# Kernel tuning notes

Measured on AMD Instinct MI355X. Metric: run time of the kernel, lower is better.

Reference implementation:

```python
import jax, jax.numpy as jnp
import numpy as np

B, IN_DIM, D, H, L = 16, 4096, 100, 200, 4
N, E = B * IN_DIM, 8 * B * IN_DIM
EPS = 1e-7  # GENConv message eps


def setup_inputs() -> dict:
    key = jax.random.key(0)
    ks = jax.random.split(key, 16)
    s = 0.05
    return {
        "x": jax.random.normal(ks[0], (N, 1), jnp.float32),
        "edge_index": jax.random.randint(ks[1], (2, E), 0, N),
        "batch_ids": jnp.repeat(jnp.arange(B), IN_DIM),  # graphs of exactly IN_DIM nodes
        "enc_w": jax.random.normal(ks[2], (1, D), jnp.float32) * s,
        "enc_b": jnp.zeros((D,), jnp.float32),
        "h1_w": jax.random.normal(ks[3], (IN_DIM, 1000), jnp.float32) * 0.02,
        "h1_b": jnp.zeros((1000,), jnp.float32),
        "h2_w": jax.random.normal(ks[4], (1000, 100), jnp.float32) * s,
        "h2_b": jnp.zeros((100,), jnp.float32),
        "ln_g": jnp.ones((L, D), jnp.float32),
        "ln_b": jnp.zeros((L, D), jnp.float32),
        "w1": jax.random.normal(ks[5], (L, D, H), jnp.float32) * s,
        "b1": jnp.zeros((L, H), jnp.float32),
        "bn_g": jnp.ones((L, H), jnp.float32),
        "bn_b": jnp.zeros((L, H), jnp.float32),
        "w2": jax.random.normal(ks[6], (L, H, D), jnp.float32) * s,
        "b2": jnp.zeros((L, D), jnp.float32),
        "dec_w": jax.random.normal(ks[7], (D, 1), jnp.float32) * s,
        "dec_b": jnp.zeros((1,), jnp.float32),
    }


def reference(x, edge_index, batch_ids, enc_w, enc_b, h1_w, h1_b, h2_w, h2_b,
              ln_g, ln_b, w1, b1, bn_g, bn_b, w2, b2, dec_w, dec_b):
    src, dst = edge_index[0], edge_index[1]
    # dense branch: [B, IN_DIM] -> 1000 -> 100 with leaky_relu (dropout p=0)
    xs = x.reshape(B, IN_DIM)
    xs = jax.nn.leaky_relu(xs @ h1_w + h1_b, 0.01)
    xs = jax.nn.leaky_relu(xs @ h2_w + h2_b, 0.01)

    h = x @ enc_w + enc_b  # node encoder -> [N, D]
    for i in range(L):  # DeepGCNLayer res+: x + GENConv(dropout(relu(LN(x))))
        mu = jnp.mean(h, axis=-1, keepdims=True)
        var = jnp.mean((h - mu) ** 2, axis=-1, keepdims=True)
        hn = (h - mu) * jax.lax.rsqrt(var + 1e-5) * ln_g[i] + ln_b[i]
        hn = jnp.maximum(hn, 0.0)  # act (dropout in eval mode = identity)
        # GENConv: message = relu(x_j) + eps, softmax aggregation (t=1)
        m = jnp.maximum(hn[src], 0.0) + EPS            # [E, D]
        mx = jax.ops.segment_max(m, dst, num_segments=N)
        ex = jnp.exp(m - mx[dst])
        den = jax.ops.segment_sum(ex, dst, num_segments=N)
        agg = jax.ops.segment_sum((ex / den[dst]) * m, dst, num_segments=N)
        # out = mlp(agg + x): Linear(D,2D) -> BN(eval) -> ReLU -> Linear(2D,D)
        z = (agg + hn) @ w1[i] + b1[i]
        z = jnp.maximum(z * bn_g[i] + bn_b[i], 0.0)
        h = h + (z @ w2[i] + b2[i])

    pooled = jax.ops.segment_sum(h, batch_ids, num_segments=B) / IN_DIM
    out = 0.5 * xs + 0.5 * pooled
    return (out @ dec_w + dec_b)[:, 0]
```

## Files before the change

kernel.cpp:

```cpp
#include <hip/hip_runtime.h>
#include <hip/hip_bf16.h>
#include <hip/hip_fp16.h>
#include <math.h>

#define B_ 16
#define IN_DIM_ 4096
#define D_ 100
#define H_ 200
#define L_ 4
#define N_ (B_*IN_DIM_)
#define E_ (8*B_*IN_DIM_)
#define EPS_ 1e-7f

typedef __attribute__((ext_vector_type(8))) short bf16x8s;
typedef __attribute__((ext_vector_type(4))) float f32x4;

__device__ inline unsigned pack_bf16x2(float a, float b){
  __hip_bfloat16 x = __float2bfloat16(a), y = __float2bfloat16(b);
  unsigned short ux = *(unsigned short*)&x, uy = *(unsigned short*)&y;
  return (unsigned)ux | ((unsigned)uy << 16);
}
__device__ inline __half2 u2h(unsigned v){ return *(__half2*)&v; }

__device__ inline unsigned char f2fp8(float v){
  unsigned p = __builtin_amdgcn_cvt_pk_fp8_f32(v, 0.f, 0u, false);
  return (unsigned char)(p & 0xFF);
}

__global__ void enc_stats_kernel(const float* __restrict__ enc_w,
                                 const float* __restrict__ enc_b,
                                 float* __restrict__ stats) {
  __shared__ float sw[128], sb[128], sww[128], swb[128], sbb[128];
  int t = threadIdx.x;
  float w=0.f, b=0.f;
  if (t < D_){ w = enc_w[t]; b = enc_b[t]; }
  sw[t]=w; sb[t]=b; sww[t]=w*w; swb[t]=w*b; sbb[t]=b*b;
  __syncthreads();
  for (int off=64; off; off>>=1){
    if (t<off){ sw[t]+=sw[t+off]; sb[t]+=sb[t+off]; sww[t]+=sww[t+off];
                swb[t]+=swb[t+off]; sbb[t]+=sbb[t+off]; }
    __syncthreads();
  }
  if (t==0){
    float mw = sw[0]*(1.f/D_), mb = sb[0]*(1.f/D_);
    stats[0]=mw; stats[1]=mb;
    stats[2]=sww[0]*(1.f/D_) - mw*mw;
    stats[3]=swb[0]*(1.f/D_) - mw*mb;
    stats[4]=sbb[0]*(1.f/D_) - mb*mb;
  }
}

#define D1_BLKS_   512
#define ENC_BLKS_  2048
#define DEG_BLKS_  2048
#define PREP_BLKS_ 448
#define SETUP_BLKS_ (D1_BLKS_+ENC_BLKS_+DEG_BLKS_+PREP_BLKS_)

__global__ void setup_kernel(const float* __restrict__ x, const float* __restrict__ enc_w,
                             const float* __restrict__ enc_b, const float* __restrict__ g0,
                             const float* __restrict__ b0, const float* __restrict__ stats,
                             __half* __restrict__ h, char* __restrict__ hnb,
                             char* __restrict__ hnb8,
                             const int* __restrict__ dsts, int* __restrict__ deg,
                             const float* __restrict__ h1_w, float* __restrict__ xs1acc,
                             const float* __restrict__ w1, const float* __restrict__ w2,
                             __hip_bfloat16* __restrict__ w1T, char* __restrict__ w2T8) {
  __shared__ float xl[16][32];
  int bid = blockIdx.x;
  int t = threadIdx.x;
  if (bid < D1_BLKS_) {
    int bx = bid & 3, by = bid >> 2;
    int k0 = by * 32;
    for (int i = t; i < 16*32; i += 256) {
      int b = i >> 5, kk = i & 31;
      xl[b][kk] = x[b*IN_DIM_ + k0 + kk];
    }
    __syncthreads();
    int c = bx*256 + t;
    if (c >= 1000) return;
    float acc[B_];
    #pragma unroll
    for (int b=0;b<B_;b++) acc[b]=0.f;
    #pragma unroll 4
    for (int kk=0; kk<32; kk++) {
      float w = h1_w[(size_t)(k0+kk)*1000 + c];
      #pragma unroll
      for (int b=0;b<B_;b++) acc[b] += xl[b][kk]*w;
    }
    #pragma unroll
    for (int b=0;b<B_;b++) atomicAdd(&xs1acc[b*1000+c], acc[b]);
  } else if (bid < D1_BLKS_+ENC_BLKS_) {
    int eb = bid - D1_BLKS_;
    int wave = t >> 6, lane = t & 63;
    int base = eb*32 + wave*8;
    float mw = stats[0], mb = stats[1], vw = stats[2], cwb = stats[3], vb = stats[4];
    float xv = 0.f;
    if (lane < 8) xv = x[base + lane];
    int c0 = 2*lane, c1 = c0+1;
    bool v = c0 < D_;
    float ew0=0.f, ew1=0.f, ebv0=0.f, ebv1=0.f, gg0=0.f, gg1=0.f, bv0=0.f, bv1=0.f;
    if (v) { ew0=enc_w[c0]; ew1=enc_w[c1]; ebv0=enc_b[c0]; ebv1=enc_b[c1];
             gg0=g0[c0]; gg1=g0[c1]; bv0=b0[c0]; bv1=b0[c1]; }
    #pragma unroll
    for (int it=0; it<8; ++it) {
      int wid = base + it;
      float xn = __shfl(xv, it, 64);
      float mu = fmaf(xn, mw, mb);
      float var = fmaf(xn*xn, vw, fmaf(2.f*xn, cwb, vb));
      float rstd = rsqrtf(var + 1e-5f);
      float h0 = fmaf(xn, ew0, ebv0);
      float h1 = fmaf(xn, ew1, ebv1);
      if (c0 < 112) *(__half2*)&h[(size_t)wid*112 + c0] = __floats2half2_rn(h0, h1);
      float n0 = v? fmaxf(fmaf((h0-mu)*rstd, gg0, bv0), 0.f) : 0.f;
      float n1 = v? fmaxf(fmaf((h1-mu)*rstd, gg1, bv1), 0.f) : 0.f;
      *(__half2*)(hnb + (size_t)wid*256 + 4*lane) = __floats2half2_rn(n0, n1);
      unsigned short p8 = (unsigned short)f2fp8(n0) | ((unsigned short)f2fp8(n1) << 8);
      *(unsigned short*)(hnb8 + (size_t)wid*128 + c0) = p8;
    }
  } else if (bid < D1_BLKS_+ENC_BLKS_+DEG_BLKS_) {
    int e = (bid - (D1_BLKS_+ENC_BLKS_))*256 + t;
    if (e < E_) atomicAdd(&deg[dsts[e]], 1);
  } else {
    int idx = (bid - (D1_BLKS_+ENC_BLKS_+DEG_BLKS_))*256 + t;
    if (idx < L_*224*128) {
      int l = idx / (224*128);
      int rem = idx % (224*128);
      int col = rem / 128, k = rem % 128;
      float v = (col < H_ && k < D_) ? w1[(l*D_ + k)*H_ + col] : 0.f;
      w1T[idx] = __float2bfloat16(v);
    }
    if (idx < L_*112*224) {
      int l = idx / (112*224);
      int rem = idx % (112*224);
      int col = rem / 224, k = rem % 224;
      float v = (col < D_ && k < H_) ? w2[(l*H_ + k)*D_ + col] : 0.f;
      w2T8[idx] = f2fp8(v);
    }
  }
}

__global__ void stage2_kernel(const int* __restrict__ deg, int* __restrict__ row_start,
                              const float* __restrict__ xs1acc, const float* __restrict__ h1_b,
                              const float* __restrict__ h2_w, float* __restrict__ xs2acc,
                              int* __restrict__ hist) {
  __shared__ int sums[1024];
  int t = threadIdx.x;
  int bid = blockIdx.x;
  if (bid == 0) {
    int base = t*64;
    int s = 0;
    for (int j=0;j<64;j++) s += deg[base+j];
    sums[t] = s;
    __syncthreads();
    for (int off=1; off<1024; off<<=1){
      int add = (t>=off)? sums[t-off] : 0;
      __syncthreads();
      sums[t] += add;
      __syncthreads();
    }
    int excl = (t==0)? 0 : sums[t-1];
    int run = excl;
    for (int j=0;j<64;j++){ row_start[base+j] = run; run += deg[base+j]; }
    if (t==1023) row_start[N_] = run;
  } else if (bid <= 4) {
    int T = (bid-1)*1024 + t;
    if (T >= 100*40) return;
    int c = T % 100, kc = T / 100;
    int k0 = kc*25;
    float acc[B_];
    #pragma unroll
    for (int b=0;b<B_;b++) acc[b]=0.f;
    for (int kk=0;kk<25;kk++){
      int k = k0+kk;
      float w = h2_w[k*100 + c];
      float bk = h1_b[k];
      #pragma unroll
      for (int b=0;b<B_;b++){
        float m = xs1acc[b*1000+k] + bk;
        m = (m>0.f)? m : 0.01f*m;
        acc[b] += m*w;
      }
    }
    #pragma unroll
    for (int b=0;b<B_;b++) atomicAdd(&xs2acc[b*100+c], acc[b]);
  } else {
    __shared__ int lh[256];
    if (t < 256) lh[t] = 0;
    __syncthreads();
    int base = (bid-5)*16384;
    for (int n = base + t; n < base + 16384; n += 1024) {
      int d = deg[n]; if (d > 255) d = 255;
      atomicAdd(&lh[d], 1);
    }
    __syncthreads();
    if (t < 256 && lh[t] > 0) atomicAdd(&hist[t], lh[t]);
  }
}

__global__ void binscan_kernel(const int* __restrict__ hist, int* __restrict__ binoff,
                               int* __restrict__ bincnt) {
  __shared__ int s[256];
  int t = threadIdx.x;
  int hv = hist[t];
  s[t] = hv;
  __syncthreads();
  for (int off=1; off<256; off<<=1){
    int v = (t>=off)? s[t-off] : 0;
    __syncthreads();
    s[t] += v;
    __syncthreads();
  }
  binoff[t] = s[t] - hv;
  bincnt[t] = 0;
}

__global__ void scatter_kernel(const int* __restrict__ srcs, const int* __restrict__ dst,
                               const int* __restrict__ row_start, int* __restrict__ cnt,
                               int* __restrict__ sorted_src,
                               const int* __restrict__ deg, const int* __restrict__ binoff,
                               int* __restrict__ bincnt, int* __restrict__ order) {
  int bid = blockIdx.x;
  int t = threadIdx.x;
  if (bid < 2048) {
    int e = bid*256 + t;
    int d = dst[e];
    int p = row_start[d] + atomicAdd(&cnt[d], 1);
    sorted_src[p] = srcs[e];
  } else {
    __shared__ int lh[256], lbase[256];
    int n = (bid-2048)*256 + t;
    int d = deg[n]; int b = (d > 255) ? 255 : d;
    lh[t] = 0;
    __syncthreads();
    int myrank = atomicAdd(&lh[b], 1);
    __syncthreads();
    lbase[t] = (lh[t] > 0) ? atomicAdd(&bincnt[t], lh[t]) : 0;
    __syncthreads();
    order[binoff[b] + lbase[b] + myrank] = n;
  }
}

__global__ void agg_kernel(const char* __restrict__ hnb, const char* __restrict__ hnb8,
                           const int* __restrict__ row_start,
                           const int* __restrict__ sorted_src,
                           const int* __restrict__ order, unsigned* __restrict__ u) {
  int gw = (blockIdx.x*256 + threadIdx.x) >> 6;
  int lane = threadIdx.x & 63;
  int lpos = lane & 31;
  int gbase = lane & 32;
  int node = order[gw*2 + (lane >> 5)];
  int beg = row_start[node];
  int deg = row_start[node+1] - beg;
  int dother = __shfl_xor(deg, 32, 64);
  int mdeg = deg > dother ? deg : dother;
  const char* lanep8 = hnb8 + 4*lpos;
  float s0=0.f,s1=0.f,s2=0.f,s3=0.f, w0=0.f,w1=0.f,w2=0.f,w3=0.f;

#define CONSUME_(R) { \
    float v0=__builtin_amdgcn_cvt_f32_fp8(R,0)+EPS_; \
    float v1=__builtin_amdgcn_cvt_f32_fp8(R,1)+EPS_; \
    float v2=__builtin_amdgcn_cvt_f32_fp8(R,2)+EPS_; \
    float v3=__builtin_amdgcn_cvt_f32_fp8(R,3)+EPS_; \
    float e0=__expf(v0), e1=__expf(v1), e2=__expf(v2), e3=__expf(v3); \
    s0+=e0; w0=fmaf(e0,v0,w0); s1+=e1; w1=fmaf(e1,v1,w1); \
    s2+=e2; w2=fmaf(e2,v2,w2); s3+=e3; w3=fmaf(e3,v3,w3); }

  for (int cb=0; cb<mdeg; cb+=32){
    int cidx = (cb + lpos < deg) ? sorted_src[beg + cb + lpos] : 0;
    int cnt = mdeg - cb; if (cnt > 32) cnt = 32;
    int grem = deg - cb;
    int glim = grem < cnt ? grem : cnt; if (glim < 0) glim = 0;
    unsigned r0=0, r1=0, r2=0, r3=0;
    if (0 < glim) r0 = *(const unsigned*)(lanep8 + (size_t)__shfl(cidx, gbase+0)*128);
    if (1 < glim) r1 = *(const unsigned*)(lanep8 + (size_t)__shfl(cidx, gbase+1)*128);
    if (2 < glim) r2 = *(const unsigned*)(lanep8 + (size_t)__shfl(cidx, gbase+2)*128);
    if (3 < glim) r3 = *(const unsigned*)(lanep8 + (size_t)__shfl(cidx, gbase+3)*128);
    for (int j=0; j<cnt; j+=4){
      unsigned n0=0, n1=0, n2=0, n3=0;
      if (j+4 < glim) n0 = *(const unsigned*)(lanep8 + (size_t)__shfl(cidx, gbase+j+4)*128);
      if (j+5 < glim) n1 = *(const unsigned*)(lanep8 + (size_t)__shfl(cidx, gbase+j+5)*128);
      if (j+6 < glim) n2 = *(const unsigned*)(lanep8 + (size_t)__shfl(cidx, gbase+j+6)*128);
      if (j+7 < glim) n3 = *(const unsigned*)(lanep8 + (size_t)__shfl(cidx, gbase+j+7)*128);
      if (j   < glim) CONSUME_(r0);
      if (j+1 < glim) CONSUME_(r1);
      if (j+2 < glim) CONSUME_(r2);
      if (j+3 < glim) CONSUME_(r3);
      r0=n0; r1=n1; r2=n2; r3=n3;
    }
  }
#undef CONSUME_

  uint2 own = *(const uint2*)(hnb + (size_t)node*256 + 8*lpos);
  __half2 oa = u2h(own.x), ob = u2h(own.y);
  float u0 = ((deg>0)? w0/s0 : 0.f) + __low2float(oa);
  float u1 = ((deg>0)? w1/s1 : 0.f) + __high2float(oa);
  float u2 = ((deg>0)? w2/s2 : 0.f) + __low2float(ob);
  float u3 = ((deg>0)? w3/s3 : 0.f) + __high2float(ob);
  if (lpos >= 25) { u0=0.f; u1=0.f; u2=0.f; u3=0.f; }
  uint2 outv; outv.x = pack_bf16x2(u0,u1); outv.y = pack_bf16x2(u2,u3);
  *(uint2*)((char*)u + (size_t)node*256 + 8*lpos) = outv;
}

__global__ __launch_bounds__(256,4) void gemm1_kernel(
    const char* __restrict__ u, const __hip_bfloat16* __restrict__ w1T,
    const float* __restrict__ b1, const float* __restrict__ bng, const float* __restrict__ bnb,
    char* __restrict__ z8) {
  __shared__ __align__(16) char wL[112*272];
  int bid = blockIdx.x;
  int half = bid & 1;
  size_t row0 = (size_t)(bid >> 1) * 64;
  int t = threadIdx.x;
  const char* wg = (const char*)w1T + (size_t)half*112*256;
  #pragma unroll
  for (int c = t; c < 1792; c += 256) {
    int r = c >> 4, sb = (c & 15) << 4;
    *(float4*)(wL + r*272 + sb) = *(const float4*)(wg + (size_t)r*256 + sb);
  }
  __syncthreads();
  int wave = t >> 6, lane = t & 63;
  int l15 = lane & 15;
  int kgb = (lane >> 4) << 4;
  int ar = wave*16 + l15;
  bf16x8s a[4];
  #pragma unroll
  for (int ks=0; ks<4; ks++)
    a[ks] = *(const bf16x8s*)(u + (row0 + ar)*256 + ks*64 + kgb);
  f32x4 acc[7];
  #pragma unroll
  for (int n=0;n<7;n++) acc[n] = (f32x4){0.f,0.f,0.f,0.f};
  #pragma unroll
  for (int ks=0; ks<4; ks++) {
    int kb = ks*64 + kgb;
    #pragma unroll
    for (int n=0;n<7;n++) {
      bf16x8s b = *(const bf16x8s*)(wL + (n*16 + l15)*272 + kb);
      acc[n] = __builtin_amdgcn_mfma_f32_16x16x32_bf16(a[ks], b, acc[n], 0, 0, 0);
    }
  }
  size_t rbase = row0 + wave*16 + ((lane>>4)<<2);
  #pragma unroll
  for (int n=0;n<7;n++) {
    int col = half*112 + n*16 + l15;
    float bias = (col < H_) ? b1[col] : 0.f;
    float g    = (col < H_) ? bng[col] : 0.f;
    float bb   = (col < H_) ? bnb[col] : 0.f;
    #pragma unroll
    for (int r=0;r<4;r++) {
      float v = fmaxf((acc[n][r] + bias)*g + bb, 0.f);
      if (col >= H_) v = 0.f;
      *(unsigned char*)(z8 + (rbase + r)*224 + col) = f2fp8(v);
    }
  }
}

template<int LAST>
__global__ __launch_bounds__(256,4) void gemm2_kernel(
    const char* __restrict__ z8, const char* __restrict__ w2T8,
    const float* __restrict__ b2, __half* __restrict__ h,
    const float* __restrict__ lng, const float* __restrict__ lnb,
    char* __restrict__ hnb, char* __restrict__ hnb8, float* __restrict__ pooled) {
  __shared__ __align__(16) char wL[112*232];
  int t = threadIdx.x;
  size_t row0 = (size_t)blockIdx.x * 64;
  const char* wg = w2T8;
  for (int c = t; c < 1568; c += 256) {
    int r = c / 14, sb = (c - r*14) << 4;
    *(float4*)(wL + r*232 + sb) = *(const float4*)(wg + (size_t)r*224 + sb);
  }
  __syncthreads();
  int wave = t >> 6, lane = t & 63;
  int l15 = lane & 15;
  int g8 = (lane >> 4) << 3;
  int ar = wave*16 + l15;
  long long av[7];
  {
    const char* zrow = z8 + (row0 + ar)*224;
    #pragma unroll
    for (int ks=0; ks<7; ks++)
      av[ks] = *(const long long*)(zrow + ks*32 + g8);
  }
  f32x4 acc[7];
  #pragma unroll
  for (int n=0;n<7;n++) acc[n] = (f32x4){0.f,0.f,0.f,0.f};
  #pragma unroll
  for (int ks=0; ks<7; ks++) {
    int kb = ks*32 + g8;
    #pragma unroll
    for (int n=0;n<7;n++) {
      long long bv = *(const long long*)(wL + (n*16 + l15)*232 + kb);
      acc[n] = __builtin_amdgcn_mfma_f32_16x16x32_fp8_fp8(av[ks], bv, acc[n], 0, 0, 0);
    }
  }
  size_t rbase = row0 + wave*16 + ((lane>>4)<<2);

  float x_[7][4];
  float sum[4]  = {0,0,0,0};
  float sum2[4] = {0,0,0,0};
  float psum[7] = {0,0,0,0,0,0,0};
  #pragma unroll
  for (int n=0;n<7;n++) {
    int col = n*16 + l15;
    bool valid = col < D_;
    float bias = valid ? b2[col] : 0.f;
    #pragma unroll
    for (int r=0;r<4;r++) {
      float xv = 0.f;
      if (valid) xv = acc[n][r] + bias + __half2float(h[(rbase + r)*112 + col]);
      x_[n][r] = xv;
      if (LAST) {
        psum[n] += xv;
      } else {
        sum[r] += xv; sum2[r] += xv*xv;
        if (valid) h[(rbase + r)*112 + col] = __float2half(xv);
      }
    }
  }

  if (LAST) {
    #pragma unroll
    for (int n=0;n<7;n++) {
      psum[n] += __shfl_xor(psum[n], 16, 64);
      psum[n] += __shfl_xor(psum[n], 32, 64);
    }
    __syncthreads();
    float* ps = (float*)wL;
    if (lane < 16) {
      #pragma unroll
      for (int n=0;n<7;n++) ps[wave*112 + n*16 + l15] = psum[n];
    }
    __syncthreads();
    if (t < D_) {
      float v = ps[t] + ps[112+t] + ps[224+t] + ps[336+t];
      int b = (int)(row0 >> 12);
      atomicAdd(&pooled[b*D_ + t], v);
    }
  } else {
    #pragma unroll
    for (int r=0;r<4;r++) {
      float s = sum[r], s2 = sum2[r];
      #pragma unroll
      for (int m=1;m<16;m<<=1) { s += __shfl_xor(s, m, 16); s2 += __shfl_xor(s2, m, 16); }
      sum[r] = s; sum2[r] = s2;
    }
    #pragma unroll
    for (int n=0;n<7;n++) {
      int col = n*16 + l15;
      float g  = (col < D_) ? lng[col] : 0.f;
      float be = (col < D_) ? lnb[col] : 0.f;
      #pragma unroll
      for (int r=0;r<4;r++) {
        float mu = sum[r]*(1.f/D_);
        float var = sum2[r]*(1.f/D_) - mu*mu;
        float rstd = rsqrtf(var + 1e-5f);
        float hv = fmaxf(fmaf((x_[n][r]-mu)*rstd, g, be), 0.f);
        if (col >= D_) hv = 0.f;
        *(__half*)(hnb + (rbase + r)*256 + 2*col) = __float2half(hv);
        *(unsigned char*)(hnb8 + (rbase + r)*128 + col) = f2fp8(hv);
      }
    }
    {
      int col = 112 + l15;
      __half zh = __float2half(0.f);
      #pragma unroll
      for (int r=0;r<4;r++) {
        *(__half*)(hnb + (rbase + r)*256 + 2*col) = zh;
        *(unsigned char*)(hnb8 + (rbase + r)*128 + col) = 0;
      }
    }
  }
}

__global__ void final_kernel(const float* __restrict__ xs2acc, const float* __restrict__ h2_b,
                             const float* __restrict__ pooled,
                             const float* __restrict__ dec_w, const float* __restrict__ dec_b,
                             float* __restrict__ out) {
  __shared__ float red[128];
  int t = threadIdx.x;
  for (int b=0;b<B_;b++){
    float v = 0.f;
    if (t < D_) {
      float xs = xs2acc[b*D_+t] + h2_b[t];
      xs = (xs>0.f)? xs : 0.01f*xs;
      v = (0.5f*xs + (0.5f/IN_DIM_)*pooled[b*D_+t]) * dec_w[t];
    }
    red[t] = v;
    __syncthreads();
    for (int off=64; off; off>>=1){
      if (t < off) red[t] += red[t+off];
      __syncthreads();
    }
    if (t==0) out[b] = red[0] + dec_b[0];
    __syncthreads();
  }
}

extern "C" void kernel_launch(void* const* d_in, const int* in_sizes, int n_in,
                              void* d_out, int out_size, void* d_ws, size_t ws_size,
                              hipStream_t stream) {
  const float* x      = (const float*)d_in[0];
  const int*   eidx   = (const int*)d_in[1];
  const float* enc_w  = (const float*)d_in[3];
  const float* enc_b  = (const float*)d_in[4];
  const float* h1_w   = (const float*)d_in[5];
  const float* h1_b   = (const float*)d_in[6];
  const float* h2_w   = (const float*)d_in[7];
  const float* h2_b   = (const float*)d_in[8];
  const float* ln_g   = (const float*)d_in[9];
  const float* ln_b   = (const float*)d_in[10];
  const float* w1     = (const float*)d_in[11];
  const float* b1     = (const float*)d_in[12];
  const float* bn_g   = (const float*)d_in[13];
  const float* bn_b   = (const float*)d_in[14];
  const float* w2     = (const float*)d_in[15];
  const float* b2     = (const float*)d_in[16];
  const float* dec_w  = (const float*)d_in[17];
  const float* dec_b  = (const float*)d_in[18];
  float* out = (float*)d_out;

  char* ws = (char*)d_ws;
  size_t off = 0;
  auto alloc = [&](size_t bytes)->char* {
    char* p = ws + off;
    off += (bytes + 255) & ~(size_t)255;
    return p;
  };
  __half* h     = (__half*)alloc((size_t)N_*112*2);
  char*  hnb    = alloc((size_t)N_*256);
  char*  hnb8   = alloc((size_t)N_*128);
  char*  z8     = alloc((size_t)N_*224);
  unsigned* u   = (unsigned*)alloc((size_t)N_*64*4);
  __hip_bfloat16* w1T = (__hip_bfloat16*)alloc((size_t)L_*224*128*2);
  char* w2T8    = alloc((size_t)L_*112*224);
  size_t zbsz = 64000 + 6400 + 6400 + (size_t)N_*4 + (size_t)N_*4 + 1024;
  char* zb = alloc(zbsz);
  float* xs1    = (float*)zb;
  float* xs2    = (float*)(zb + 64000);
  float* pooled = (float*)(zb + 64000 + 6400);
  int* deg      = (int*)(zb + 64000 + 6400 + 6400);
  int* cnt      = (int*)(zb + 64000 + 6400 + 6400 + (size_t)N_*4);
  int* hist     = (int*)(zb + 64000 + 6400 + 6400 + (size_t)N_*8);
  int* row_start  = (int*)alloc((N_+1)*4);
  int* sorted_src = (int*)alloc((size_t)E_*4);
  int* order      = (int*)alloc((size_t)N_*4);
  int* binoff     = (int*)alloc(1024);
  int* bincnt     = (int*)alloc(1024);
  float* stats    = (float*)alloc(256);

  const int* srcs = eidx;
  const int* dsts = eidx + E_;

  hipMemsetAsync(zb, 0, zbsz, stream);

  enc_stats_kernel<<<1, 128, 0, stream>>>(enc_w, enc_b, stats);
  setup_kernel<<<SETUP_BLKS_, 256, 0, stream>>>(x, enc_w, enc_b, ln_g, ln_b, stats,
                                                h, hnb, hnb8,
                                                dsts, deg, h1_w, xs1, w1, w2, w1T, w2T8);
  stage2_kernel<<<9, 1024, 0, stream>>>(deg, row_start, xs1, h1_b, h2_w, xs2, hist);
  binscan_kernel<<<1, 256, 0, stream>>>(hist, binoff, bincnt);
  scatter_kernel<<<2048+256, 256, 0, stream>>>(srcs, dsts, row_start, cnt, sorted_src,
                                               deg, binoff, bincnt, order);

  for (int i=0;i<L_;i++){
    agg_kernel<<<N_/8, 256, 0, stream>>>(hnb, hnb8, row_start, sorted_src, order, u);
    gemm1_kernel<<<(N_/64)*2, 256, 0, stream>>>((const char*)u,
                                                w1T + (size_t)i*224*128, b1 + i*H_,
                                                bn_g + i*H_, bn_b + i*H_, z8);
    if (i < L_-1) {
      gemm2_kernel<0><<<N_/64, 256, 0, stream>>>(z8, w2T8 + (size_t)i*112*224, b2 + i*D_,
                                                 h, ln_g + (i+1)*D_, ln_b + (i+1)*D_,
                                                 hnb, hnb8, pooled);
    } else {
      gemm2_kernel<1><<<N_/64, 256, 0, stream>>>(z8, w2T8 + (size_t)i*112*224, b2 + i*D_,
                                                 h, nullptr, nullptr, hnb, hnb8, pooled);
    }
  }

  final_kernel<<<1, 128, 0, stream>>>(xs2, h2_b, pooled, dec_w, dec_b, out);
}
```

Measured before the change: 365.3 us.

## Fuse softmax aggregation into first MLP GEMM via shared-memory tile

Merges the aggregation and first GEMM kernels so each block aggregates 16 degree-ordered nodes into a bf16 tile in shared memory, then runs MFMA against w1T read directly from global memory and scatters fp8 outputs to the original node rows. This removes the global round-trip of the intermediate u buffer and one launch per layer. Aggregation now uses 16 lanes per node with 8-byte loads instead of 32 lanes with 4-byte loads. The trade-offs are a smaller GEMM tile (16 rows) with weights re-read from global/L2 per block, and scattered byte stores to z8.

```diff
diff --git a/kernel.cpp b/kernel.cpp
--- a/kernel.cpp
+++ b/kernel.cpp
@@ -240,115 +240,126 @@
   }
 }
 
-__global__ void agg_kernel(const char* __restrict__ hnb, const char* __restrict__ hnb8,
-                           const int* __restrict__ row_start,
-                           const int* __restrict__ sorted_src,
-                           const int* __restrict__ order, unsigned* __restrict__ u) {
-  int gw = (blockIdx.x*256 + threadIdx.x) >> 6;
-  int lane = threadIdx.x & 63;
-  int lpos = lane & 31;
-  int gbase = lane & 32;
-  int node = order[gw*2 + (lane >> 5)];
+__global__ __launch_bounds__(256,4) void agg_gemm1_kernel(
+    const char* __restrict__ hnb, const char* __restrict__ hnb8,
+    const int* __restrict__ row_start, const int* __restrict__ sorted_src,
+    const int* __restrict__ order,
+    const __hip_bfloat16* __restrict__ w1T, const float* __restrict__ b1,
+    const float* __restrict__ bng, const float* __restrict__ bnb,
+    char* __restrict__ z8) {
+  __shared__ __align__(16) char uL[16*272];
+  __shared__ int ord_l[16];
+  int t = threadIdx.x;
+  int wave = t >> 6, lane = t & 63;
+  if (t < 16) ord_l[t] = order[blockIdx.x*16 + t];
+  int lpos = lane & 15;
+  int grp  = lane >> 4;
+  int gbase = lane & 48;
+  int idxb = wave*4 + grp;
+  int node = order[blockIdx.x*16 + idxb];
   int beg = row_start[node];
   int deg = row_start[node+1] - beg;
-  int dother = __shfl_xor(deg, 32, 64);
-  int mdeg = deg > dother ? deg : dother;
-  const char* lanep8 = hnb8 + 4*lpos;
-  float s0=0.f,s1=0.f,s2=0.f,s3=0.f, w0=0.f,w1=0.f,w2=0.f,w3=0.f;
-
-#define CONSUME_(R) { \
-    float v0=__builtin_amdgcn_cvt_f32_fp8(R,0)+EPS_; \
-    float v1=__builtin_amdgcn_cvt_f32_fp8(R,1)+EPS_; \
-    float v2=__builtin_amdgcn_cvt_f32_fp8(R,2)+EPS_; \
-    float v3=__builtin_amdgcn_cvt_f32_fp8(R,3)+EPS_; \
+  int m1 = __shfl_xor(deg, 16, 64); int mdeg = deg > m1 ? deg : m1;
+  m1 = __shfl_xor(mdeg, 32, 64); mdeg = mdeg > m1 ? mdeg : m1;
+  const char* lanep8 = hnb8 + 8*lpos;
+  float s0=0.f,s1=0.f,s2=0.f,s3=0.f,s4=0.f,s5=0.f,s6=0.f,s7=0.f;
+  float w0=0.f,w1v=0.f,w2v=0.f,w3=0.f,w4=0.f,w5=0.f,w6=0.f,w7=0.f;
+
+#define CONSUME8_(R) { \
+    float v0=__builtin_amdgcn_cvt_f32_fp8(R.x,0)+EPS_; \
+    float v1=__builtin_amdgcn_cvt_f32_fp8(R.x,1)+EPS_; \
+    float v2=__builtin_amdgcn_cvt_f32_fp8(R.x,2)+EPS_; \
+    float v3=__builtin_amdgcn_cvt_f32_fp8(R.x,3)+EPS_; \
+    float v4=__builtin_amdgcn_cvt_f32_fp8(R.y,0)+EPS_; \
+    float v5=__builtin_amdgcn_cvt_f32_fp8(R.y,1)+EPS_; \
+    float v6=__builtin_amdgcn_cvt_f32_fp8(R.y,2)+EPS_; \
+    float v7=__builtin_amdgcn_cvt_f32_fp8(R.y,3)+EPS_; \
     float e0=__expf(v0), e1=__expf(v1), e2=__expf(v2), e3=__expf(v3); \
-    s0+=e0; w0=fmaf(e0,v0,w0); s1+=e1; w1=fmaf(e1,v1,w1); \
-    s2+=e2; w2=fmaf(e2,v2,w2); s3+=e3; w3=fmaf(e3,v3,w3); }
-
-  for (int cb=0; cb<mdeg; cb+=32){
+    float e4=__expf(v4), e5=__expf(v5), e6=__expf(v6), e7=__expf(v7); \
+    s0+=e0; w0 =fmaf(e0,v0,w0);  s1+=e1; w1v=fmaf(e1,v1,w1v); \
+    s2+=e2; w2v=fmaf(e2,v2,w2v); s3+=e3; w3 =fmaf(e3,v3,w3); \
+    s4+=e4; w4 =fmaf(e4,v4,w4);  s5+=e5; w5 =fmaf(e5,v5,w5); \
+    s6+=e6; w6 =fmaf(e6,v6,w6);  s7+=e7; w7 =fmaf(e7,v7,w7); }
+
+  for (int cb=0; cb<mdeg; cb+=16){
     int cidx = (cb + lpos < deg) ? sorted_src[beg + cb + lpos] : 0;
-    int cnt = mdeg - cb; if (cnt > 32) cnt = 32;
+    int cnt = mdeg - cb; if (cnt > 16) cnt = 16;
     int grem = deg - cb;
     int glim = grem < cnt ? grem : cnt; if (glim < 0) glim = 0;
-    unsigned r0=0, r1=0, r2=0, r3=0;
-    if (0 < glim) r0 = *(const unsigned*)(lanep8 + (size_t)__shfl(cidx, gbase+0)*128);
-    if (1 < glim) r1 = *(const unsigned*)(lanep8 + (size_t)__shfl(cidx, gbase+1)*128);
-    if (2 < glim) r2 = *(const unsigned*)(lanep8 + (size_t)__shfl(cidx, gbase+2)*128);
-    if (3 < glim) r3 = *(const unsigned*)(lanep8 + (size_t)__shfl(cidx, gbase+3)*128);
+    uint2 r0={0,0}, r1={0,0}, r2={0,0}, r3={0,0};
+    if (0 < glim) r0 = *(const uint2*)(lanep8 + (size_t)__shfl(cidx, gbase+0)*128);
+    if (1 < glim) r1 = *(const uint2*)(lanep8 + (size_t)__shfl(cidx, gbase+1)*128);
+    if (2 < glim) r2 = *(const uint2*)(lanep8 + (size_t)__shfl(cidx, gbase+2)*128);
+    if (3 < glim) r3 = *(const uint2*)(lanep8 + (size_t)__shfl(cidx, gbase+3)*128);
     for (int j=0; j<cnt; j+=4){
-      unsigned n0=0, n1=0, n2=0, n3=0;
-      if (j+4 < glim) n0 = *(const unsigned*)(lanep8 + (size_t)__shfl(cidx, gbase+j+4)*128);
-      if (j+5 < glim) n1 = *(const unsigned*)(lanep8 + (size_t)__shfl(cidx, gbase+j+5)*128);
-      if (j+6 < glim) n2 = *(const unsigned*)(lanep8 + (size_t)__shfl(cidx, gbase+j+6)*128);
-      if (j+7 < glim) n3 = *(const unsigned*)(lanep8 + (size_t)__shfl(cidx, gbase+j+7)*128);
-      if (j   < glim) CONSUME_(r0);
-      if (j+1 < glim) CONSUME_(r1);
-      if (j+2 < glim) CONSUME_(r2);
-      if (j+3 < glim) CONSUME_(r3);
+      uint2 n0={0,0}, n1={0,0}, n2={0,0}, n3={0,0};
+      if (j+4 < glim) n0 = *(const uint2*)(lanep8 + (size_t)__shfl(cidx, gbase+j+4)*128);
+      if (j+5 < glim) n1 = *(const uint2*)(lanep8 + (size_t)__shfl(cidx, gbase+j+5)*128);
+      if (j+6 < glim) n2 = *(const uint2*)(lanep8 + (size_t)__shfl(cidx, gbase+j+6)*128);
+      if (j+7 < glim) n3 = *(const uint2*)(lanep8 + (size_t)__shfl(cidx, gbase+j+7)*128);
+      if (j   < glim) CONSUME8_(r0);
+      if (j+1 < glim) CONSUME8_(r1);
+      if (j+2 < glim) CONSUME8_(r2);
+      if (j+3 < glim) CONSUME8_(r3);
       r0=n0; r1=n1; r2=n2; r3=n3;
     }
   }
-#undef CONSUME_
-
-  uint2 own = *(const uint2*)(hnb + (size_t)node*256 + 8*lpos);
-  __half2 oa = u2h(own.x), ob = u2h(own.y);
-  float u0 = ((deg>0)? w0/s0 : 0.f) + __low2float(oa);
-  float u1 = ((deg>0)? w1/s1 : 0.f) + __high2float(oa);
-  float u2 = ((deg>0)? w2/s2 : 0.f) + __low2float(ob);
-  float u3 = ((deg>0)? w3/s3 : 0.f) + __high2float(ob);
-  if (lpos >= 25) { u0=0.f; u1=0.f; u2=0.f; u3=0.f; }
-  uint2 outv; outv.x = pack_bf16x2(u0,u1); outv.y = pack_bf16x2(u2,u3);
-  *(uint2*)((char*)u + (size_t)node*256 + 8*lpos) = outv;
-}
-
-__global__ __launch_bounds__(256,4) void gemm1_kernel(
-    const char* __restrict__ u, const __hip_bfloat16* __restrict__ w1T,
-    const float* __restrict__ b1, const float* __restrict__ bng, const float* __restrict__ bnb,
-    char* __restrict__ z8) {
-  __shared__ __align__(16) char wL[112*272];
-  int bid = blockIdx.x;
-  int half = bid & 1;
-  size_t row0 = (size_t)(bid >> 1) * 64;
-  int t = threadIdx.x;
-  const char* wg = (const char*)w1T + (size_t)half*112*256;
-  #pragma unroll
-  for (int c = t; c < 1792; c += 256) {
-    int r = c >> 4, sb = (c & 15) << 4;
-    *(float4*)(wL + r*272 + sb) = *(const float4*)(wg + (size_t)r*256 + sb);
+#undef CONSUME8_
+
+  {
+    uint4 sv = *(const uint4*)(hnb + (size_t)node*256 + lpos*16);
+    __half2 ha = u2h(sv.x), hb = u2h(sv.y), hc = u2h(sv.z), hd = u2h(sv.w);
+    float inv = (deg>0)? 1.f : 0.f;
+    float q0 = (deg>0? w0 /s0 :0.f) + __low2float(ha);
+    float q1 = (deg>0? w1v/s1 :0.f) + __high2float(ha);
+    float q2 = (deg>0? w2v/s2 :0.f) + __low2float(hb);
+    float q3 = (deg>0? w3 /s3 :0.f) + __high2float(hb);
+    float q4 = (deg>0? w4 /s4 :0.f) + __low2float(hc);
+    float q5 = (deg>0? w5 /s5 :0.f) + __high2float(hc);
+    float q6 = (deg>0? w6 /s6 :0.f) + __low2float(hd);
+    float q7 = (deg>0? w7 /s7 :0.f) + __high2float(hd);
+    (void)inv;
+    int c0 = lpos*8;
+    if (c0+0 >= D_) q0 = 0.f;
+    if (c0+1 >= D_) q1 = 0.f;
+    if (c0+2 >= D_) q2 = 0.f;
+    if (c0+3 >= D_) q3 = 0.f;
+    if (c0+4 >= D_) q4 = 0.f;
+    if (c0+5 >= D_) q5 = 0.f;
+    if (c0+6 >= D_) q6 = 0.f;
+    if (c0+7 >= D_) q7 = 0.f;
+    unsigned* up = (unsigned*)(uL + idxb*272 + lpos*16);
+    up[0] = pack_bf16x2(q0,q1);
+    up[1] = pack_bf16x2(q2,q3);
+    up[2] = pack_bf16x2(q4,q5);
+    up[3] = pack_bf16x2(q6,q7);
   }
   __syncthreads();
-  int wave = t >> 6, lane = t & 63;
+
   int l15 = lane & 15;
   int kgb = (lane >> 4) << 4;
-  int ar = wave*16 + l15;
   bf16x8s a[4];
   #pragma unroll
   for (int ks=0; ks<4; ks++)
-    a[ks] = *(const bf16x8s*)(u + (row0 + ar)*256 + ks*64 + kgb);
-  f32x4 acc[7];
-  #pragma unroll
-  for (int n=0;n<7;n++) acc[n] = (f32x4){0.f,0.f,0.f,0.f};
-  #pragma unroll
-  for (int ks=0; ks<4; ks++) {
-    int kb = ks*64 + kgb;
-    #pragma unroll
-    for (int n=0;n<7;n++) {
-      bf16x8s b = *(const bf16x8s*)(wL + (n*16 + l15)*272 + kb);
-      acc[n] = __builtin_amdgcn_mfma_f32_16x16x32_bf16(a[ks], b, acc[n], 0, 0, 0);
-    }
-  }
-  size_t rbase = row0 + wave*16 + ((lane>>4)<<2);
-  #pragma unroll
-  for (int n=0;n<7;n++) {
-    int col = half*112 + n*16 + l15;
+    a[ks] = *(const bf16x8s*)(uL + l15*272 + ks*64 + kgb);
+  for (int n = wave; n < 14; n += 4) {
+    f32x4 acc = (f32x4){0.f,0.f,0.f,0.f};
+    const char* wrow = (const char*)w1T + (size_t)(n*16 + l15)*256;
+    #pragma unroll
+    for (int ks=0; ks<4; ks++) {
+      bf16x8s b = *(const bf16x8s*)(wrow + ks*64 + kgb);
+      acc = __builtin_amdgcn_mfma_f32_16x16x32_bf16(a[ks], b, acc, 0, 0, 0);
+    }
+    int col = n*16 + l15;
     float bias = (col < H_) ? b1[col] : 0.f;
     float g    = (col < H_) ? bng[col] : 0.f;
     float bb   = (col < H_) ? bnb[col] : 0.f;
     #pragma unroll
     for (int r=0;r<4;r++) {
-      float v = fmaxf((acc[n][r] + bias)*g + bb, 0.f);
+      float v = fmaxf((acc[r] + bias)*g + bb, 0.f);
       if (col >= H_) v = 0.f;
-      *(unsigned char*)(z8 + (rbase + r)*224 + col) = f2fp8(v);
+      int row = ord_l[((lane>>4)<<2) + r];
+      *(unsigned char*)(z8 + (size_t)row*224 + col) = f2fp8(v);
     }
   }
 }
@@ -528,7 +539,6 @@
   char*  hnb    = alloc((size_t)N_*256);
   char*  hnb8   = alloc((size_t)N_*128);
   char*  z8     = alloc((size_t)N_*224);
-  unsigned* u   = (unsigned*)alloc((size_t)N_*64*4);
   __hip_bfloat16* w1T = (__hip_bfloat16*)alloc((size_t)L_*224*128*2);
   char* w2T8    = alloc((size_t)L_*112*224);
   size_t zbsz = 64000 + 6400 + 6400 + (size_t)N_*4 + (size_t)N_*4 + 1024;
@@ -561,8 +571,7 @@
                                                deg, binoff, bincnt, order);
 
   for (int i=0;i<L_;i++){
-    agg_kernel<<<N_/8, 256, 0, stream>>>(hnb, hnb8, row_start, sorted_src, order, u);
-    gemm1_kernel<<<(N_/64)*2, 256, 0, stream>>>((const char*)u,
+    agg_gemm1_kernel<<<N_/16, 256, 0, stream>>>(hnb, hnb8, row_start, sorted_src, order,
                                                 w1T + (size_t)i*224*128, b1 + i*H_,
                                                 bn_g + i*H_, bn_b + i*H_, z8);
     if (i < L_-1) {
```

Measured after the change: 377.9 us. 1.03x slower.
